# Kernel optimization log

Hardware: AMD Instinct MI355X
Metric: run time of the kernel (lower is better)

Reference implementation:

```python
import jax, jax.numpy as jnp
import numpy as np

INPUT, HIDDEN, OUTPUT, LAYERS = 256, 512, 256, 2


def _lstm_cell(x, h, c, Wih, Whh, bih, bhh):
    # gates in torch order: i, f, g, o  -> [B, 4H]
    g = x @ Wih.T + bih + h @ Whh.T + bhh
    i, f, gg, o = jnp.split(g, 4, axis=-1)
    c_new = jax.nn.sigmoid(f) * c + jax.nn.sigmoid(i) * jnp.tanh(gg)
    h_new = jax.nn.sigmoid(o) * jnp.tanh(c_new)
    return h_new, c_new


def setup_inputs() -> dict:
    key = jax.random.key(0)
    ks = jax.random.split(key, 16)
    s = 0.05
    inp = {
        "z0": jax.random.normal(ks[0], (1024, INPUT), jnp.float32),
        "h0": jax.random.normal(ks[1], (LAYERS, 1024, HIDDEN), jnp.float32),
        "c0": jax.random.normal(ks[2], (LAYERS, 1024, HIDDEN), jnp.float32),
        # layer 0: input_size -> hidden
        "W_ih0": jax.random.normal(ks[3], (4 * HIDDEN, INPUT), jnp.float32) * s,
        "W_hh0": jax.random.normal(ks[4], (4 * HIDDEN, HIDDEN), jnp.float32) * s,
        "b_ih0": jax.random.normal(ks[5], (4 * HIDDEN,), jnp.float32) * s,
        "b_hh0": jax.random.normal(ks[6], (4 * HIDDEN,), jnp.float32) * s,
        # layer 1: hidden -> hidden
        "W_ih1": jax.random.normal(ks[7], (4 * HIDDEN, HIDDEN), jnp.float32) * s,
        "W_hh1": jax.random.normal(ks[8], (4 * HIDDEN, HIDDEN), jnp.float32) * s,
        "b_ih1": jax.random.normal(ks[9], (4 * HIDDEN,), jnp.float32) * s,
        "b_hh1": jax.random.normal(ks[10], (4 * HIDDEN,), jnp.float32) * s,
        # fc: hidden -> input (feedback), linear: input -> output
        "fc_W": jax.random.normal(ks[11], (INPUT, HIDDEN), jnp.float32) * s,
        "fc_b": jax.random.normal(ks[12], (INPUT,), jnp.float32) * s,
        "lin_W": jax.random.normal(ks[13], (OUTPUT, INPUT), jnp.float32) * s,
        "lin_b": jax.random.normal(ks[14], (OUTPUT,), jnp.float32) * s,
        "T2": 128,
    }
    return inp


def reference(z0, h0, c0, W_ih0, W_hh0, b_ih0, b_hh0,
              W_ih1, W_hh1, b_ih1, b_hh1, fc_W, fc_b, lin_W, lin_b, T2):
    params = [(W_ih0, W_hh0, b_ih0, b_hh0), (W_ih1, W_hh1, b_ih1, b_hh1)]

    def step(carry, _):
        z, h, c = carry          # z:[B,in], h/c:[L,B,H]
        x = z
        hs, cs = [], []
        for l, (Wih, Whh, bih, bhh) in enumerate(params):
            hn, cn = _lstm_cell(x, h[l], c[l], Wih, Whh, bih, bhh)
            hs.append(hn); cs.append(cn)
            x = hn
        z_new = x @ fc_W.T + fc_b
        return (z_new, jnp.stack(hs), jnp.stack(cs)), z_new

    _, zs = jax.lax.scan(step, (z0, h0, c0), None, length=T2)  # [T2,B,in]
    return zs @ lin_W.T + lin_b  # [T2, B, output]
```

## Files before the change

### kernel.cpp

```cpp
#include <hip/hip_runtime.h>


typedef __attribute__((ext_vector_type(8))) __bf16 bf16x8;
typedef __attribute__((ext_vector_type(16))) float f32x16;
typedef unsigned long long ull;

__device__ __forceinline__ f32x16 mfma_bf16(bf16x8 a, bf16x8 b, f32x16 c) {
  return __builtin_amdgcn_mfma_f32_32x32x16_bf16(a, b, c, 0, 0, 0);
}

__device__ __forceinline__ short f2bf(float f) {
  unsigned u = __float_as_uint(f);
  u += 0x7fffu + ((u >> 16) & 1u);
  return (short)(u >> 16);
}

__device__ __forceinline__ float sigm(float x) { return 1.0f / (1.0f + __expf(-x)); }
__device__ __forceinline__ float tanh_fast(float x) { return 2.0f / (1.0f + __expf(-2.0f * x)) - 1.0f; }

__device__ __forceinline__ f32x16 zero16() {
  f32x16 z;
#pragma unroll
  for (int i = 0; i < 16; ++i) z[i] = 0.0f;
  return z;
}

__device__ __forceinline__ void dma16(const void* g, void* l) {
  __builtin_amdgcn_global_load_lds(
      (const __attribute__((address_space(1))) void*)g,
      (__attribute__((address_space(3))) void*)l, 16, 0, 0);
}

#define AT_STRIDE 132

__global__ __launch_bounds__(256) void prep_kernel(
    const float* __restrict__ z0, const float* __restrict__ h0in,
    const float* __restrict__ Wih0, const float* __restrict__ Whh0,
    const float* __restrict__ bih0, const float* __restrict__ bhh0,
    const float* __restrict__ Wih1, const float* __restrict__ Whh1,
    const float* __restrict__ bih1, const float* __restrict__ bhh1,
    const float* __restrict__ fcW, const float* __restrict__ linW,
    short* __restrict__ wsw0, short* __restrict__ wsw1,
    short* __restrict__ fcWsw, short* __restrict__ linWsw,
    float* __restrict__ bias0, float* __restrict__ bias1,
    short* __restrict__ zb1, short* __restrict__ h0b0, short* __restrict__ h1b0,
    int* __restrict__ flags)
{
  int idx = blockIdx.x * 256 + threadIdx.x;
  if (idx < 1572864) {
    int jj = idx & 7, l = (idx >> 3) & 63, gg = (idx >> 9) & 3;
    int rest = idx >> 11;
    int s = rest % 48, b = rest / 48;
    int row = gg * 512 + b * 32 + (l & 31);
    int k = s * 16 + (l >> 5) * 8 + jj;
    wsw0[idx] = f2bf(k < 512 ? Whh0[row * 512 + k] : Wih0[row * 256 + (k - 512)]);
    return;
  }
  idx -= 1572864;
  if (idx < 2097152) {
    int jj = idx & 7, l = (idx >> 3) & 63, gg = (idx >> 9) & 3;
    int rest = idx >> 11;
    int s = rest & 63, b = rest >> 6;
    int row = gg * 512 + b * 32 + (l & 31);
    int k = s * 16 + (l >> 5) * 8 + jj;
    wsw1[idx] = f2bf(k < 512 ? Whh1[row * 512 + k] : Wih1[row * 512 + (k - 512)]);
    return;
  }
  idx -= 2097152;
  if (idx < 131072) {
    int jj = idx & 7, l = (idx >> 3) & 63, s = (idx >> 9) & 31, jz = idx >> 14;
    int col = jz * 32 + (l & 31);
    int k = s * 16 + (l >> 5) * 8 + jj;
    fcWsw[idx] = f2bf(fcW[col * 512 + k]);
    return;
  }
  idx -= 131072;
  if (idx < 65536) {
    int jj = idx & 7, l = (idx >> 3) & 63, s = (idx >> 9) & 15, jo = idx >> 13;
    int col = jo * 32 + (l & 31);
    int k = s * 16 + (l >> 5) * 8 + jj;
    linWsw[idx] = f2bf(linW[col * 256 + k]);
    return;
  }
  idx -= 65536;
  if (idx < 2048) { bias0[idx] = bih0[idx] + bhh0[idx]; return; }
  idx -= 2048;
  if (idx < 2048) { bias1[idx] = bih1[idx] + bhh1[idx]; return; }
  idx -= 2048;
  if (idx < 262144) { zb1[idx] = f2bf(z0[idx]); return; }
  idx -= 262144;
  if (idx < 524288) { h0b0[idx] = f2bf(h0in[idx]); return; }
  idx -= 524288;
  if (idx < 524288) { h1b0[idx] = f2bf(h0in[524288 + idx]); return; }
  idx -= 524288;
  if (idx < 8448) {
    int v = 0;
    if (idx < 8192) {
      int off = idx & 255;
      if (off == 32) v = 8;
      else if (off == 64 || off == 128) v = 16;
    }
    flags[idx] = v;
    return;
  }
}

__device__ __forceinline__ void wait1(int* c0, int v0) {
  __syncthreads();
  if (threadIdx.x == 0) {
    while (__hip_atomic_load(c0, __ATOMIC_RELAXED, __HIP_MEMORY_SCOPE_AGENT) < v0)
      __builtin_amdgcn_s_sleep(2);
    asm volatile("buffer_inv" ::: "memory");
  }
  __syncthreads();
}

__device__ __forceinline__ void wait2(int* c0, int v0, int* c1, int v1) {
  __syncthreads();
  if (threadIdx.x == 0) {
    while (__hip_atomic_load(c0, __ATOMIC_RELAXED, __HIP_MEMORY_SCOPE_AGENT) < v0 ||
           __hip_atomic_load(c1, __ATOMIC_RELAXED, __HIP_MEMORY_SCOPE_AGENT) < v1)
      __builtin_amdgcn_s_sleep(2);
    asm volatile("buffer_inv" ::: "memory");
  }
  __syncthreads();
}

__device__ __forceinline__ void produce(int* c) {
  asm volatile("s_waitcnt vmcnt(0)" ::: "memory");
  __syncthreads();
  if (threadIdx.x == 0)
    __hip_atomic_fetch_add(c, 1, __ATOMIC_RELAXED, __HIP_MEMORY_SCOPE_AGENT);
}

__device__ __forceinline__ void cell_warm(short* Bl, const short* __restrict__ wgl) {
  __syncthreads();
  const int t = threadIdx.x, w = t >> 6;
#pragma unroll
  for (int g = 0; g < 6; ++g)
#pragma unroll
    for (int i = 0; i < 2; ++i)
      dma16(wgl + (size_t)g * 8192 + (i * 512 + t) * 8,
            Bl + g * 8192 + i * 4096 + w * 512);
}

__device__ __forceinline__ void proA3(short* Al, const short* __restrict__ srcA,
                                      int ldA, int row0) {
  const int t = threadIdx.x, w = t >> 6, l = t & 63;
#pragma unroll
  for (int g = 0; g < 3; ++g)
    dma16(srcA + (size_t)(row0 + l) * ldA + g * 64 + w * 8,
          Al + g * 4096 + w * 512);
}

template <int NG, int TAG>
__device__ __forceinline__ void cell_phase_dma(
    short* Al, short* Bl, float* gbuf,
    const short* __restrict__ srcA, int ldA,
    const short* __restrict__ srcB, int ldB,
    const short* __restrict__ wgl,
    const float (&br)[4][4],
    float* cr, short* hout, int row0, int j0)
{
  const int t = threadIdx.x;
  const int w = t >> 6, l = t & 63;
  const int gq = w >> 1, mh = w & 1;
  const int ln = l & 31, kh = l >> 5;

  auto issueA = [&](int g) {
    const short* asrc; int ald, gk;
    if (g < TAG) { asrc = srcA; ald = ldA; gk = g * 64; }
    else         { asrc = srcB; ald = ldB; gk = (g - TAG) * 64; }
    const short* gp = asrc + (size_t)(row0 + l) * ald + gk + w * 8;
    dma16(gp, Al + (g % 3) * 4096 + w * 512);
  };
  auto issueB = [&](int g) {
    const short* gb = wgl + (size_t)g * 8192;
    short* lb = Bl + (g % 6) * 8192;
#pragma unroll
    for (int i = 0; i < 2; ++i)
      dma16(gb + (i * 512 + t) * 8, lb + i * 4096 + w * 512);
  };

  f32x16 acc = zero16();

#pragma unroll
  for (int g = 0; g < NG; ++g) {
    if (g == 0)           asm volatile("s_waitcnt vmcnt(2)" ::: "memory");
    else if (g == 1)      asm volatile("s_waitcnt vmcnt(4)" ::: "memory");
    else if (g == 2)      asm volatile("s_waitcnt vmcnt(6)" ::: "memory");
    else if (g + 6 <= NG) asm volatile("s_waitcnt vmcnt(8)" ::: "memory");
    else if (g + 5 == NG) asm volatile("s_waitcnt vmcnt(6)" ::: "memory");
    else if (g + 4 == NG) asm volatile("s_waitcnt vmcnt(4)" ::: "memory");
    else if (g + 3 == NG) asm volatile("s_waitcnt vmcnt(2)" ::: "memory");
    else if (g + 2 == NG) asm volatile("s_waitcnt vmcnt(1)" ::: "memory");
    else                  asm volatile("s_waitcnt vmcnt(0)" ::: "memory");
    __builtin_amdgcn_s_barrier();
    __builtin_amdgcn_sched_barrier(0);
    const short* al = Al + (g % 3) * 4096;
    const short* bl = Bl + (g % 6) * 8192;
#pragma unroll
    for (int u = 0; u < 4; ++u) {
      bf16x8 a = *(const bf16x8*)&al[((u * 2 + kh) * 64 + mh * 32 + ln) * 8];
      bf16x8 b = *(const bf16x8*)&bl[((u * 4 + gq) * 64 + l) * 8];
      acc = mfma_bf16(a, b, acc);
    }
    __builtin_amdgcn_sched_barrier(0);
    __builtin_amdgcn_s_barrier();
    __builtin_amdgcn_sched_barrier(0);
    if (g + 3 < NG) issueA(g + 3);
    if (g + 6 < NG) issueB(g + 6);
  }

#pragma unroll
  for (int r = 0; r < 16; ++r) {
    int mloc = (r & 3) + 8 * (r >> 2) + 4 * kh + mh * 32;
    gbuf[(gq * 64 + mloc) * 32 + ln] = acc[r];
  }
  __syncthreads();
  const int m = t >> 3, nb = (t & 7) * 4;
  short hh[4];
#pragma unroll
  for (int u = 0; u < 4; ++u) {
    int n = nb + u;
    float gi = gbuf[(0 * 64 + m) * 32 + n] + br[0][u];
    float gf = gbuf[(1 * 64 + m) * 32 + n] + br[1][u];
    float gg = gbuf[(2 * 64 + m) * 32 + n] + br[2][u];
    float go = gbuf[(3 * 64 + m) * 32 + n] + br[3][u];
    float cn = sigm(gf) * cr[u] + sigm(gi) * tanh_fast(gg);
    cr[u] = cn;
    hh[u] = f2bf(sigm(go) * tanh_fast(cn));
  }
  ull hv; __builtin_memcpy(&hv, hh, 8);
  *(ull*)&hout[(size_t)(row0 + m) * 512 + j0 + nb] = hv;
}

template <int NQ>
__device__ __forceinline__ void proj_partials(
    short* At0, float* gbuf,
    const short* __restrict__ src, int ld,
    const short* __restrict__ wblk, int row0)
{
  const int t = threadIdx.x;
  const int w = t >> 6, l = t & 63;
  const int kq = w >> 1, mh = w & 1;
  const int ln = l & 31, kh = l >> 5;
  const int sks = t & 15, sm = t >> 4;
  f32x16 acc = zero16();
  uint4 pre[NQ][2];
  bf16x8 bfr[NQ][2];
#pragma unroll
  for (int q = 0; q < NQ; ++q) {
#pragma unroll
    for (int i = 0; i < 2; ++i)
      pre[q][i] = *(const uint4*)&src[(row0 + sm + 32 * i) * ld + q * 128 + sks * 8];
#pragma unroll
    for (int sl = 0; sl < 2; ++sl)
      bfr[q][sl] = *(const bf16x8*)&wblk[((q * 8 + kq * 2 + sl) * 64 + l) * 8];
  }
#pragma unroll
  for (int q = 0; q < NQ; ++q) {
    __syncthreads();
#pragma unroll
    for (int i = 0; i < 2; ++i)
      *(uint4*)&At0[(sm + 32 * i) * AT_STRIDE + sks * 8] = pre[q][i];
    __syncthreads();
#pragma unroll
    for (int sl = 0; sl < 2; ++sl) {
      int s16 = kq * 2 + sl;
      bf16x8 a = *(const bf16x8*)&At0[(mh * 32 + ln) * AT_STRIDE + (s16 * 2 + kh) * 8];
      acc = mfma_bf16(a, bfr[q][sl], acc);
    }
  }
  __syncthreads();
#pragma unroll
  for (int r = 0; r < 16; ++r) {
    int mloc = (r & 3) + 8 * (r >> 2) + 4 * kh + mh * 32;
    gbuf[(kq * 64 + mloc) * 32 + ln] = acc[r];
  }
  __syncthreads();
}

__global__ __launch_bounds__(512, 1) void decoder_persist(
    const short* __restrict__ wsw0, const short* __restrict__ wsw1,
    const short* __restrict__ fcWsw, const short* __restrict__ linWsw,
    const float* __restrict__ bias0, const float* __restrict__ bias1,
    const float* __restrict__ fcb, const float* __restrict__ linb,
    const float* __restrict__ c0in,
    short* h0x, short* h0y, short* h1x, short* h1y, short* zx, short* zy,
    int* flags, float* __restrict__ outp)
{
  __shared__ __align__(16) short Al[12288];
  __shared__ __align__(16) short Bl[49152];
  __shared__ int sgj[2];
  float* gbuf = (float*)Bl;
  short* Atp = Bl;
  float* gbufp = (float*)(Bl + 8448);

  if (threadIdx.x == 0) {
    unsigned xcc;
    asm volatile("s_getreg_b32 %0, hwreg(HW_REG_XCC_ID, 0, 32)" : "=s"(xcc));
    xcc &= 7u;
    int slot = __hip_atomic_fetch_add(&flags[8192 + (int)xcc * 32], 1,
                                      __ATOMIC_RELAXED, __HIP_MEMORY_SCOPE_AGENT);
    slot &= 31;
    sgj[0] = (int)xcc * 2 + (slot >> 4);
    sgj[1] = slot & 15;
  }
  __syncthreads();
  const int g = sgj[0], j = sgj[1];
  const int row0 = g * 64, j0 = j * 32;
  int* cnt = &flags[g * 256];
#define CZ(i)  (cnt + (0 + (i)) * 32)
#define CH0(i) (cnt + (2 + (i)) * 32)
#define CH1(i) (cnt + (4 + (i)) * 32)

  float c0r[4], c1r[4], b0r[4][4], b1r[4][4], fbr[4];
  {
    const int m = threadIdx.x >> 3, nb = (threadIdx.x & 7) * 4;
#pragma unroll
    for (int u = 0; u < 4; ++u) {
      c0r[u] = c0in[(size_t)(row0 + m) * 512 + j0 + nb + u];
      c1r[u] = c0in[524288 + (size_t)(row0 + m) * 512 + j0 + nb + u];
      int jn = j0 + nb + u;
#pragma unroll
      for (int gt = 0; gt < 4; ++gt) {
        b0r[gt][u] = bias0[gt * 512 + jn];
        b1r[gt][u] = bias1[gt * 512 + jn];
      }
      fbr[u] = (j < 8) ? fcb[j * 32 + nb + u] : linb[(j - 8) * 32 + nb + u];
    }
  }

  short* h0buf[2] = {h0x, h0y};
  short* h1buf[2] = {h1x, h1y};
  short* zbuf[2] = {zx, zy};
  const short* wg0 = wsw0 + j * 98304;
  const short* wg1 = wsw1 + j * 131072;
  const short* wpj = (j < 8) ? (fcWsw + j * 16384) : (linWsw + (j - 8) * 8192);

#pragma unroll 1
  for (int t = 0; t < 128; ++t) {
    const int p = t & 1;
    const int half = (t >> 1) + 1;
    const int full = (t + 3) >> 1;
    cell_warm(Bl, wg0);
    proA3(Al, h0buf[p], 512, row0);
    wait2(CZ(p ^ 1), 8 * half, CH0(p), 16 * half);
    cell_phase_dma<12, 8>(Al, Bl, gbuf, h0buf[p], 512, zbuf[p ^ 1], 256,
                          wg0, b0r, c0r, h0buf[p ^ 1], row0, j0);
    produce(CH0(p ^ 1));
    cell_warm(Bl, wg1);
    if (j < 8) {
      proA3(Al, h1buf[p], 512, row0);
      wait2(CH0(p ^ 1), 16 * full, CH1(p), 16 * half);
    } else {
      wait2(CH0(p ^ 1), 16 * full, CH1(p), 16 * half);
      proA3(Al, h1buf[p], 512, row0);
    }
    cell_phase_dma<16, 8>(Al, Bl, gbuf, h1buf[p], 512, h0buf[p ^ 1], 512,
                          wg1, b1r, c1r, h1buf[p ^ 1], row0, j0);
    produce(CH1(p ^ 1));
    if (j < 8) {
      wait1(CH1(p ^ 1), 16 * full);
      proj_partials<4>(Atp, gbufp, h1buf[p ^ 1], 512, wpj, row0);
      const int m = threadIdx.x >> 3, nb = (threadIdx.x & 7) * 4;
      const int n0 = j * 32;
      short zz[4];
#pragma unroll
      for (int u = 0; u < 4; ++u) {
        int n = nb + u;
        float v = gbufp[(0 * 64 + m) * 32 + n] + gbufp[(1 * 64 + m) * 32 + n] +
                  gbufp[(2 * 64 + m) * 32 + n] + gbufp[(3 * 64 + m) * 32 + n] +
                  fbr[u];
        zz[u] = f2bf(v);
      }
      ull zv; __builtin_memcpy(&zv, zz, 8);
      *(ull*)&zbuf[p][(size_t)(row0 + m) * 256 + n0 + nb] = zv;
      produce(CZ(p));
    } else if (t > 0) {
      proj_partials<2>(Atp, gbufp, zbuf[p ^ 1], 256, wpj, row0);
      const int m = threadIdx.x >> 3, nb = (threadIdx.x & 7) * 4;
      const int n0 = (j - 8) * 32;
      float4 ov;
      float* po = &ov.x;
#pragma unroll
      for (int u = 0; u < 4; ++u) {
        int n = nb + u;
        po[u] = gbufp[(0 * 64 + m) * 32 + n] + gbufp[(1 * 64 + m) * 32 + n] +
                gbufp[(2 * 64 + m) * 32 + n] + gbufp[(3 * 64 + m) * 32 + n] +
                fbr[u];
      }
      *(float4*)&outp[(size_t)(t - 1) * 262144 + (size_t)(row0 + m) * 256 + n0 + nb] = ov;
    }
  }
  if (j >= 8) {
    wait1(CZ(1), 8 * 65);
    proj_partials<2>(Atp, gbufp, zbuf[1], 256, wpj, row0);
    const int m = threadIdx.x >> 3, nb = (threadIdx.x & 7) * 4;
    const int n0 = (j - 8) * 32;
    float4 ov;
    float* po = &ov.x;
#pragma unroll
    for (int u = 0; u < 4; ++u) {
      int n = nb + u;
      po[u] = gbufp[(0 * 64 + m) * 32 + n] + gbufp[(1 * 64 + m) * 32 + n] +
              gbufp[(2 * 64 + m) * 32 + n] + gbufp[(3 * 64 + m) * 32 + n] +
              fbr[u];
    }
    *(float4*)&outp[(size_t)127 * 262144 + (size_t)(row0 + m) * 256 + n0 + nb] = ov;
  }
#undef CZ
#undef CH0
#undef CH1
}

extern "C" void kernel_launch(void* const* d_in, const int* in_sizes, int n_in,
                              void* d_out, int out_size, void* d_ws, size_t ws_size,
                              hipStream_t stream) {
  const float* z0   = (const float*)d_in[0];
  const float* h0in = (const float*)d_in[1];
  const float* c0in = (const float*)d_in[2];
  const float* Wih0 = (const float*)d_in[3];
  const float* Whh0 = (const float*)d_in[4];
  const float* bih0 = (const float*)d_in[5];
  const float* bhh0 = (const float*)d_in[6];
  const float* Wih1 = (const float*)d_in[7];
  const float* Whh1 = (const float*)d_in[8];
  const float* bih1 = (const float*)d_in[9];
  const float* bhh1 = (const float*)d_in[10];
  const float* fcW  = (const float*)d_in[11];
  const float* fcb  = (const float*)d_in[12];
  const float* linW = (const float*)d_in[13];
  const float* linb = (const float*)d_in[14];
  float* out = (float*)d_out;

  char* ws = (char*)d_ws;
  short* wsw0  = (short*)(ws + 0);
  short* wsw1  = (short*)(ws + 3145728);
  short* fcWsw = (short*)(ws + 7340032);
  short* linWsw= (short*)(ws + 7602176);
  float* bias0 = (float*)(ws + 7733248);
  float* bias1 = (float*)(ws + 7741440);
  short* zb0   = (short*)(ws + 7749632);
  short* zb1   = (short*)(ws + 8273920);
  short* h0b0  = (short*)(ws + 8798208);
  short* h0b1  = (short*)(ws + 9846784);
  short* h1b0  = (short*)(ws + 10895360);
  short* h1b1  = (short*)(ws + 11943936);
  int*   flags = (int*)  (ws + 12992512);

  prep_kernel<<<20273, 256, 0, stream>>>(z0, h0in, Wih0, Whh0, bih0, bhh0,
                                         Wih1, Whh1, bih1, bhh1, fcW, linW,
                                         wsw0, wsw1, fcWsw, linWsw, bias0, bias1,
                                         zb1, h0b0, h1b0, flags);

  decoder_persist<<<256, 512, 0, stream>>>(
      wsw0, wsw1, fcWsw, linWsw, bias0, bias1, fcb, linb, c0in,
      h0b0, h0b1, h1b0, h1b1, zb0, zb1, flags, out);
}
```

Before: 4.845 ms.

## Load LSTM cell operands directly to registers instead of LDS DMA staging

Replaces the global-to-LDS DMA pipeline for the A (hidden/input) and B (weights) operands of each LSTM cell phase with direct global loads into a 3-deep register ring. The K loop is split across wave halves, and the partial sums are reduced through a larger shared gate buffer. This removes the per-step LDS staging and the barriers inside the K loop, and lets the first prefetches start before the cross-block flag wait. In exchange it uses more VGPRs, issues more global loads per lane, and adds an extra reduction pass through LDS.

New measurement: 6.544 ms. 35.1% more time.

```diff
diff --git a/kernel.cpp b/kernel.cpp
--- a/kernel.cpp
+++ b/kernel.cpp
@@ -23,12 +23,6 @@
 #pragma unroll
   for (int i = 0; i < 16; ++i) z[i] = 0.0f;
   return z;
-}
-
-__device__ __forceinline__ void dma16(const void* g, void* l) {
-  __builtin_amdgcn_global_load_lds(
-      (const __attribute__((address_space(1))) void*)g,
-      (__attribute__((address_space(3))) void*)l, 16, 0, 0);
 }
 
 #define AT_STRIDE 132
@@ -133,89 +127,72 @@
     __hip_atomic_fetch_add(c, 1, __ATOMIC_RELAXED, __HIP_MEMORY_SCOPE_AGENT);
 }
 
-__device__ __forceinline__ void cell_warm(short* Bl, const short* __restrict__ wgl) {
-  __syncthreads();
-  const int t = threadIdx.x, w = t >> 6;
-#pragma unroll
-  for (int g = 0; g < 6; ++g)
-#pragma unroll
-    for (int i = 0; i < 2; ++i)
-      dma16(wgl + (size_t)g * 8192 + (i * 512 + t) * 8,
-            Bl + g * 8192 + i * 4096 + w * 512);
-}
-
-__device__ __forceinline__ void proA3(short* Al, const short* __restrict__ srcA,
-                                      int ldA, int row0) {
-  const int t = threadIdx.x, w = t >> 6, l = t & 63;
-#pragma unroll
-  for (int g = 0; g < 3; ++g)
-    dma16(srcA + (size_t)(row0 + l) * ldA + g * 64 + w * 8,
-          Al + g * 4096 + w * 512);
-}
-
-template <int NG, int TAG>
-__device__ __forceinline__ void cell_phase_dma(
-    short* Al, short* Bl, float* gbuf,
+template <int NG, int TAG, bool PREWAIT>
+__device__ __forceinline__ void cell_phase_reg(
+    float* gbig,
     const short* __restrict__ srcA, int ldA,
     const short* __restrict__ srcB, int ldB,
     const short* __restrict__ wgl,
     const float (&br)[4][4],
-    float* cr, short* hout, int row0, int j0)
+    float* cr, short* hout, int row0, int j0,
+    int* c0, int v0, int* c1, int v1)
 {
   const int t = threadIdx.x;
   const int w = t >> 6, l = t & 63;
-  const int gq = w >> 1, mh = w & 1;
+  const int gq = w & 3, ks = w >> 2;
   const int ln = l & 31, kh = l >> 5;
 
-  auto issueA = [&](int g) {
-    const short* asrc; int ald, gk;
-    if (g < TAG) { asrc = srcA; ald = ldA; gk = g * 64; }
-    else         { asrc = srcB; ald = ldB; gk = (g - TAG) * 64; }
-    const short* gp = asrc + (size_t)(row0 + l) * ald + gk + w * 8;
-    dma16(gp, Al + (g % 3) * 4096 + w * 512);
+  uint4 aR[3][2][2];
+  uint4 bR[3][2];
+  f32x16 acc0 = zero16(), acc1 = zero16();
+
+  auto issue = [&](int g, int slot) {
+    const short* src; int ld, gk;
+    if (g < TAG) { src = srcA; ld = ldA; gk = g * 64; }
+    else         { src = srcB; ld = ldB; gk = (g - TAG) * 64; }
+#pragma unroll
+    for (int sl = 0; sl < 2; ++sl) {
+      const int ko = gk + (ks * 2 + sl) * 16 + kh * 8;
+#pragma unroll
+      for (int mh = 0; mh < 2; ++mh)
+        aR[slot][sl][mh] =
+            *(const uint4*)&src[(size_t)(row0 + mh * 32 + ln) * ld + ko];
+      bR[slot][sl] = *(const uint4*)
+          &wgl[(size_t)g * 8192 + (((ks * 2 + sl) * 4 + gq) * 64 + l) * 8];
+    }
   };
-  auto issueB = [&](int g) {
-    const short* gb = wgl + (size_t)g * 8192;
-    short* lb = Bl + (g % 6) * 8192;
-#pragma unroll
-    for (int i = 0; i < 2; ++i)
-      dma16(gb + (i * 512 + t) * 8, lb + i * 4096 + w * 512);
-  };
-
-  f32x16 acc = zero16();
+
+  if (PREWAIT) {
+    issue(0, 0); issue(1, 1); issue(2, 2);
+    asm volatile("" ::: "memory");
+    wait2(c0, v0, c1, v1);
+  } else {
+    wait2(c0, v0, c1, v1);
+    issue(0, 0); issue(1, 1); issue(2, 2);
+  }
 
 #pragma unroll
   for (int g = 0; g < NG; ++g) {
-    if (g == 0)           asm volatile("s_waitcnt vmcnt(2)" ::: "memory");
-    else if (g == 1)      asm volatile("s_waitcnt vmcnt(4)" ::: "memory");
-    else if (g == 2)      asm volatile("s_waitcnt vmcnt(6)" ::: "memory");
-    else if (g + 6 <= NG) asm volatile("s_waitcnt vmcnt(8)" ::: "memory");
-    else if (g + 5 == NG) asm volatile("s_waitcnt vmcnt(6)" ::: "memory");
-    else if (g + 4 == NG) asm volatile("s_waitcnt vmcnt(4)" ::: "memory");
-    else if (g + 3 == NG) asm volatile("s_waitcnt vmcnt(2)" ::: "memory");
-    else if (g + 2 == NG) asm volatile("s_waitcnt vmcnt(1)" ::: "memory");
-    else                  asm volatile("s_waitcnt vmcnt(0)" ::: "memory");
-    __builtin_amdgcn_s_barrier();
-    __builtin_amdgcn_sched_barrier(0);
-    const short* al = Al + (g % 3) * 4096;
-    const short* bl = Bl + (g % 6) * 8192;
-#pragma unroll
-    for (int u = 0; u < 4; ++u) {
-      bf16x8 a = *(const bf16x8*)&al[((u * 2 + kh) * 64 + mh * 32 + ln) * 8];
-      bf16x8 b = *(const bf16x8*)&bl[((u * 4 + gq) * 64 + l) * 8];
-      acc = mfma_bf16(a, b, acc);
-    }
-    __builtin_amdgcn_sched_barrier(0);
-    __builtin_amdgcn_s_barrier();
-    __builtin_amdgcn_sched_barrier(0);
-    if (g + 3 < NG) issueA(g + 3);
-    if (g + 6 < NG) issueB(g + 6);
+    asm volatile("" ::: "memory");
+    const int slot = g % 3;
+#pragma unroll
+    for (int sl = 0; sl < 2; ++sl) {
+      bf16x8 b, a0, a1;
+      __builtin_memcpy(&b,  &bR[slot][sl],    16);
+      __builtin_memcpy(&a0, &aR[slot][sl][0], 16);
+      __builtin_memcpy(&a1, &aR[slot][sl][1], 16);
+      acc0 = mfma_bf16(a0, b, acc0);
+      acc1 = mfma_bf16(a1, b, acc1);
+    }
+    asm volatile("" ::: "memory");
+    if (g + 3 < NG) issue(g + 3, slot);
   }
 
 #pragma unroll
   for (int r = 0; r < 16; ++r) {
-    int mloc = (r & 3) + 8 * (r >> 2) + 4 * kh + mh * 32;
-    gbuf[(gq * 64 + mloc) * 32 + ln] = acc[r];
+    int mloc = (r & 3) + 8 * (r >> 2) + 4 * kh;
+    gbig[ks * 8192 + (gq * 64 + mloc) * 32 + ln] = acc0[r];
+    gbig[ks * 8192 + (gq * 64 + mloc + 32) * 32 + ln] = acc1[r];
   }
   __syncthreads();
   const int m = t >> 3, nb = (t & 7) * 4;
@@ -223,10 +200,10 @@
 #pragma unroll
   for (int u = 0; u < 4; ++u) {
     int n = nb + u;
-    float gi = gbuf[(0 * 64 + m) * 32 + n] + br[0][u];
-    float gf = gbuf[(1 * 64 + m) * 32 + n] + br[1][u];
-    float gg = gbuf[(2 * 64 + m) * 32 + n] + br[2][u];
-    float go = gbuf[(3 * 64 + m) * 32 + n] + br[3][u];
+    float gi = gbig[(0 * 64 + m) * 32 + n] + gbig[8192 + (0 * 64 + m) * 32 + n] + br[0][u];
+    float gf = gbig[(1 * 64 + m) * 32 + n] + gbig[8192 + (1 * 64 + m) * 32 + n] + br[1][u];
+    float gg = gbig[(2 * 64 + m) * 32 + n] + gbig[8192 + (2 * 64 + m) * 32 + n] + br[2][u];
+    float go = gbig[(3 * 64 + m) * 32 + n] + gbig[8192 + (3 * 64 + m) * 32 + n] + br[3][u];
     float cn = sigm(gf) * cr[u] + sigm(gi) * tanh_fast(gg);
     cr[u] = cn;
     hh[u] = f2bf(sigm(go) * tanh_fast(cn));
@@ -290,12 +267,10 @@
     short* h0x, short* h0y, short* h1x, short* h1y, short* zx, short* zy,
     int* flags, float* __restrict__ outp)
 {
-  __shared__ __align__(16) short Al[12288];
-  __shared__ __align__(16) short Bl[49152];
+  __shared__ __align__(16) float gbig[16384];
   __shared__ int sgj[2];
-  float* gbuf = (float*)Bl;
-  short* Atp = Bl;
-  float* gbufp = (float*)(Bl + 8448);
+  short* Atp = (short*)gbig;
+  float* gbufp = (float*)((char*)gbig + 16896);
 
   if (threadIdx.x == 0) {
     unsigned xcc;
@@ -344,22 +319,18 @@
     const int p = t & 1;
     const int half = (t >> 1) + 1;
     const int full = (t + 3) >> 1;
-    cell_warm(Bl, wg0);
-    proA3(Al, h0buf[p], 512, row0);
-    wait2(CZ(p ^ 1), 8 * half, CH0(p), 16 * half);
-    cell_phase_dma<12, 8>(Al, Bl, gbuf, h0buf[p], 512, zbuf[p ^ 1], 256,
-                          wg0, b0r, c0r, h0buf[p ^ 1], row0, j0);
+    cell_phase_reg<12, 8, true>(gbig, h0buf[p], 512, zbuf[p ^ 1], 256,
+                                wg0, b0r, c0r, h0buf[p ^ 1], row0, j0,
+                                CZ(p ^ 1), 8 * half, CH0(p), 16 * half);
     produce(CH0(p ^ 1));
-    cell_warm(Bl, wg1);
-    if (j < 8) {
-      proA3(Al, h1buf[p], 512, row0);
-      wait2(CH0(p ^ 1), 16 * full, CH1(p), 16 * half);
-    } else {
-      wait2(CH0(p ^ 1), 16 * full, CH1(p), 16 * half);
-      proA3(Al, h1buf[p], 512, row0);
-    }
-    cell_phase_dma<16, 8>(Al, Bl, gbuf, h1buf[p], 512, h0buf[p ^ 1], 512,
-                          wg1, b1r, c1r, h1buf[p ^ 1], row0, j0);
+    if (j < 8)
+      cell_phase_reg<16, 8, true>(gbig, h1buf[p], 512, h0buf[p ^ 1], 512,
+                                  wg1, b1r, c1r, h1buf[p ^ 1], row0, j0,
+                                  CH0(p ^ 1), 16 * full, CH1(p), 16 * half);
+    else
+      cell_phase_reg<16, 8, false>(gbig, h1buf[p], 512, h0buf[p ^ 1], 512,
+                                   wg1, b1r, c1r, h1buf[p ^ 1], row0, j0,
+                                   CH0(p ^ 1), 16 * full, CH1(p), 16 * half);
     produce(CH1(p ^ 1));
     if (j < 8) {
       wait1(CH1(p ^ 1), 16 * full);
```
